# Performance work log

Measured on AMD Instinct MI355X. Metric: run time of the kernel, lower is better.

## Reference

```python
import jax, jax.numpy as jnp
import numpy as np

EPS = 1e-7


def setup_inputs() -> dict:
    key = jax.random.key(0)
    k1, k2, k3, k4 = jax.random.split(key, 4)
    N, M = 8192, 8192
    inputs = jax.random.normal(k1, (N, 2), dtype=jnp.float32)
    outputs = jax.random.normal(k2, (N,), dtype=jnp.float32)
    x = jax.random.normal(k3, (M, 2), dtype=jnp.float32)
    # positive per-query bandwidths in [0.5, 1.5)
    bandwidth = 0.5 + jax.random.uniform(k4, (M,), dtype=jnp.float32)
    return {"x": x, "inputs": inputs, "outputs": outputs, "bandwidth": bandwidth}


def reference(x, inputs, outputs, bandwidth):
    # Squared pairwise distances (cdist followed by .pow(2) in the original):
    # d2[n, m] = ||inputs[n] - x[m]||^2, computed via the expansion to avoid
    # materializing an (N, M, 2) intermediate.
    a2 = jnp.sum(inputs * inputs, axis=1)  # (N,)
    b2 = jnp.sum(x * x, axis=1)            # (M,)
    d2 = a2[:, None] + b2[None, :] - 2.0 * (inputs @ x.T)  # (N, M)
    d2 = jnp.maximum(d2, 0.0)

    bw = bandwidth[None, :]  # (1, M), per-query bandwidth
    weights = jnp.exp(-d2 / (2.0 * bw * bw))  # (N, M)
    # Normalization over dim 0 (over the N reference points)
    weights = weights / (jnp.sum(weights, axis=0, keepdims=True) + EPS)
    # weights.T @ outputs -> (M,), Nadaraya-Watson weighted sum
    weighted = weights.T @ outputs  # (M,)
    return weighted
```

## Files before the change

kernel.cpp:

```cpp
#include <hip/hip_runtime.h>

#define EPS 1e-7f
#define LOG2E 1.44269504088896340736f

constexpr int BLOCK = 1024;
constexpr int JR    = 4;
constexpr int JJ    = 8;
constexpr int JB    = JJ * JR;
constexpr int SS    = BLOCK / JJ;
constexpr int CHUNK = 1024;
constexpr int PTS   = CHUNK / SS;

__global__ __launch_bounds__(BLOCK, 4) void nw_block(
    const float2* __restrict__ x,
    const float2* __restrict__ inputs,
    const float*  __restrict__ outputs,
    const float*  __restrict__ bw,
    float*        __restrict__ out,
    int N, int M)
{
    __shared__ float4 pts[SS][PTS + 1];
    __shared__ float2 red[SS][JB];

    const int tid = threadIdx.x;
    const int jj  = tid & (JJ - 1);
    const int ss  = tid >> 3;

    float c0[JR], c1[JR], c2[JR], c3[JR];
    #pragma unroll
    for (int r = 0; r < JR; ++r) {
        const int j = blockIdx.x * JB + jj + r * JJ;
        if (j < M) {
            float2 xj = x[j];
            float  b  = bw[j];
            float  k  = -LOG2E / (2.0f * b * b);
            c0[r] = k;
            c1[r] = -2.0f * k * xj.x;
            c2[r] = -2.0f * k * xj.y;
            c3[r] = k * fmaf(xj.x, xj.x, xj.y * xj.y);
        } else {
            c0[r] = c1[r] = c2[r] = c3[r] = 0.f;
        }
    }

    float num[JR], den[JR];
    #pragma unroll
    for (int r = 0; r < JR; ++r) { num[r] = 0.f; den[r] = 0.f; }

    float2 pr = make_float2(0.f, 0.f);
    float  po = 0.f;
    if (tid < min(CHUNK, N)) { pr = inputs[tid]; po = outputs[tid]; }

    for (int base = 0; base < N; base += CHUNK) {
        const int cnt = min(CHUNK, N - base);
        if (tid < cnt) {
            pts[tid >> 3][tid & (PTS - 1)] =
                make_float4(pr.x, pr.y, fmaf(pr.x, pr.x, pr.y * pr.y), po);
        } else {
            pts[tid >> 3][tid & (PTS - 1)] =
                make_float4(0.f, 0.f, 3.0e38f, 0.f);
        }
        __syncthreads();

        const int nb = base + CHUNK;
        if (nb < N) {
            const int ncnt = min(CHUNK, N - nb);
            if (tid < ncnt) { pr = inputs[nb + tid]; po = outputs[nb + tid]; }
        }

        const float4* my = pts[ss];
        #pragma unroll
        for (int l = 0; l < PTS; ++l) {
            float4 p = my[l];
            #pragma unroll
            for (int r = 0; r < JR; ++r) {
                float t = fmaf(c0[r], p.z, fmaf(c1[r], p.x, fmaf(c2[r], p.y, c3[r])));
                float w = __builtin_amdgcn_exp2f(t);
                num[r] = fmaf(w, p.w, num[r]);
                den[r] += w;
            }
        }
        __syncthreads();
    }

    #pragma unroll
    for (int r = 0; r < JR; ++r)
        red[ss][jj + r * JJ] = make_float2(num[r], den[r]);
    __syncthreads();
    if (tid < JB) {
        float n = 0.f, d = 0.f;
        for (int s = 0; s < SS; ++s) {
            n += red[s][tid].x;
            d += red[s][tid].y;
        }
        const int jo = blockIdx.x * JB + tid;
        if (jo < M) out[jo] = n / (d + EPS);
    }
}

extern "C" void kernel_launch(void* const* d_in, const int* in_sizes, int n_in,
                              void* d_out, int out_size, void* d_ws, size_t ws_size,
                              hipStream_t stream) {
    const float2* x       = (const float2*)d_in[0];
    const float2* inputs  = (const float2*)d_in[1];
    const float*  outputs = (const float*) d_in[2];
    const float*  bwv     = (const float*) d_in[3];
    const int N = in_sizes[2];
    const int M = in_sizes[3];
    float*        out     = (float*)d_out;

    dim3 grid((M + JB - 1) / JB);
    nw_block<<<grid, BLOCK, 0, stream>>>(x, inputs, outputs, bwv, out, N, M);
}
```

Measured before the change: 75.71 us.

## Use packed f32x2 math with SoA shared layout and smaller blocks

Splits the shared-memory point tile into separate x, y, squared-norm and output arrays so each thread reads pairs of points. The FMA chain and the accumulators then run on 2-wide float vectors, which lets the compiler emit packed FP32 instructions (v_pk_fma_f32). Global loads are widened to float4/float2, each covering two points. The block shrinks to 512 threads with 2 queries per thread, doubling the grid and adding parallelism, but exp2 stays scalar, so transcendental throughput may still cap the gain.

```diff
diff --git a/kernel.cpp b/kernel.cpp
--- a/kernel.cpp
+++ b/kernel.cpp
@@ -3,13 +3,16 @@
 #define EPS 1e-7f
 #define LOG2E 1.44269504088896340736f
 
-constexpr int BLOCK = 1024;
-constexpr int JR    = 4;
+typedef float f32x2 __attribute__((ext_vector_type(2)));
+
+constexpr int BLOCK = 512;
 constexpr int JJ    = 8;
+constexpr int JR    = 2;
 constexpr int JB    = JJ * JR;
 constexpr int SS    = BLOCK / JJ;
 constexpr int CHUNK = 1024;
 constexpr int PTS   = CHUNK / SS;
+constexpr int ROW   = PTS + 2;
 
 __global__ __launch_bounds__(BLOCK, 4) void nw_block(
     const float2* __restrict__ x,
@@ -19,65 +22,87 @@
     float*        __restrict__ out,
     int N, int M)
 {
-    __shared__ float4 pts[SS][PTS + 1];
+    __shared__ __align__(16) float sX[SS][ROW];
+    __shared__ __align__(16) float sY[SS][ROW];
+    __shared__ __align__(16) float sS[SS][ROW];
+    __shared__ __align__(16) float sO[SS][ROW];
     __shared__ float2 red[SS][JB];
 
     const int tid = threadIdx.x;
     const int jj  = tid & (JJ - 1);
     const int ss  = tid >> 3;
 
-    float c0[JR], c1[JR], c2[JR], c3[JR];
+    f32x2 c0p[JR], c1p[JR], c2p[JR], c3p[JR];
     #pragma unroll
     for (int r = 0; r < JR; ++r) {
         const int j = blockIdx.x * JB + jj + r * JJ;
+        float k = 0.f, v1 = 0.f, v2 = 0.f, v3 = 0.f;
         if (j < M) {
             float2 xj = x[j];
             float  b  = bw[j];
-            float  k  = -LOG2E / (2.0f * b * b);
-            c0[r] = k;
-            c1[r] = -2.0f * k * xj.x;
-            c2[r] = -2.0f * k * xj.y;
-            c3[r] = k * fmaf(xj.x, xj.x, xj.y * xj.y);
-        } else {
-            c0[r] = c1[r] = c2[r] = c3[r] = 0.f;
+            k  = -LOG2E / (2.0f * b * b);
+            v1 = -2.0f * k * xj.x;
+            v2 = -2.0f * k * xj.y;
+            v3 = k * fmaf(xj.x, xj.x, xj.y * xj.y);
         }
+        c0p[r] = {k, k}; c1p[r] = {v1, v1}; c2p[r] = {v2, v2}; c3p[r] = {v3, v3};
     }
 
-    float num[JR], den[JR];
+    f32x2 nump[JR], denp[JR];
     #pragma unroll
-    for (int r = 0; r < JR; ++r) { num[r] = 0.f; den[r] = 0.f; }
+    for (int r = 0; r < JR; ++r) { nump[r] = {0.f, 0.f}; denp[r] = {0.f, 0.f}; }
 
-    float2 pr = make_float2(0.f, 0.f);
-    float  po = 0.f;
-    if (tid < min(CHUNK, N)) { pr = inputs[tid]; po = outputs[tid]; }
+    const float4* in4  = (const float4*)inputs;
+    const float2* out2 = (const float2*)outputs;
+    float4 pin  = make_float4(0.f, 0.f, 0.f, 0.f);
+    float2 pout = make_float2(0.f, 0.f);
+    if (2 * tid + 1 < N) { pin = in4[tid]; pout = out2[tid]; }
 
     for (int base = 0; base < N; base += CHUNK) {
         const int cnt = min(CHUNK, N - base);
-        if (tid < cnt) {
-            pts[tid >> 3][tid & (PTS - 1)] =
-                make_float4(pr.x, pr.y, fmaf(pr.x, pr.x, pr.y * pr.y), po);
-        } else {
-            pts[tid >> 3][tid & (PTS - 1)] =
-                make_float4(0.f, 0.f, 3.0e38f, 0.f);
+        {
+            const int  r0 = tid >> 3;
+            const int  s0 = (2 * tid) & (PTS - 1);
+            const bool v0 = (2 * tid) < cnt;
+            const bool v1 = (2 * tid + 1) < cnt;
+            f32x2 xp = {v0 ? pin.x : 0.f, v1 ? pin.z : 0.f};
+            f32x2 yp = {v0 ? pin.y : 0.f, v1 ? pin.w : 0.f};
+            f32x2 sp = {v0 ? fmaf(pin.x, pin.x, pin.y * pin.y) : 3.0e38f,
+                        v1 ? fmaf(pin.z, pin.z, pin.w * pin.w) : 3.0e38f};
+            f32x2 op = {v0 ? pout.x : 0.f, v1 ? pout.y : 0.f};
+            *(f32x2*)&sX[r0][s0] = xp;
+            *(f32x2*)&sY[r0][s0] = yp;
+            *(f32x2*)&sS[r0][s0] = sp;
+            *(f32x2*)&sO[r0][s0] = op;
         }
         __syncthreads();
 
         const int nb = base + CHUNK;
         if (nb < N) {
-            const int ncnt = min(CHUNK, N - nb);
-            if (tid < ncnt) { pr = inputs[nb + tid]; po = outputs[nb + tid]; }
+            const int i0 = (nb >> 1) + tid;
+            if (2 * i0 + 1 < N) { pin = in4[i0]; pout = out2[i0]; }
         }
 
-        const float4* my = pts[ss];
+        const float* mx = sX[ss];
+        const float* my = sY[ss];
+        const float* ms = sS[ss];
+        const float* mo = sO[ss];
         #pragma unroll
-        for (int l = 0; l < PTS; ++l) {
-            float4 p = my[l];
+        for (int m = 0; m < PTS / 2; ++m) {
+            f32x2 xp = *(const f32x2*)&mx[2 * m];
+            f32x2 yp = *(const f32x2*)&my[2 * m];
+            f32x2 sp = *(const f32x2*)&ms[2 * m];
+            f32x2 op = *(const f32x2*)&mo[2 * m];
             #pragma unroll
             for (int r = 0; r < JR; ++r) {
-                float t = fmaf(c0[r], p.z, fmaf(c1[r], p.x, fmaf(c2[r], p.y, c3[r])));
-                float w = __builtin_amdgcn_exp2f(t);
-                num[r] = fmaf(w, p.w, num[r]);
-                den[r] += w;
+                f32x2 t = __builtin_elementwise_fma(c2p[r], yp, c3p[r]);
+                t = __builtin_elementwise_fma(c1p[r], xp, t);
+                t = __builtin_elementwise_fma(c0p[r], sp, t);
+                f32x2 w;
+                w.x = __builtin_amdgcn_exp2f(t.x);
+                w.y = __builtin_amdgcn_exp2f(t.y);
+                nump[r] = __builtin_elementwise_fma(w, op, nump[r]);
+                denp[r] += w;
             }
         }
         __syncthreads();
@@ -85,7 +110,8 @@
 
     #pragma unroll
     for (int r = 0; r < JR; ++r)
-        red[ss][jj + r * JJ] = make_float2(num[r], den[r]);
+        red[ss][jj + r * JJ] = make_float2(nump[r].x + nump[r].y,
+                                           denp[r].x + denp[r].y);
     __syncthreads();
     if (tid < JB) {
         float n = 0.f, d = 0.f;
```

New measurement: 74.12 us. -2.1%, faster.

## Stream reference points via registers with packed FMA and wave-shuffle reduction

Applied to the files above, without the earlier changes.

Replaces the LDS-staged reference-point tiling with a scheme where each thread loads its own reference points straight from global memory into registers. The FMA and accumulate math now uses two-wide float vectors, which can map to packed FP32 instructions. Each block handles 8 queries with 512 threads and reduces partial sums using wave shuffles plus a small LDS step. This removes the LDS traffic and the per-chunk barriers, at the cost of reloading each query's constants and reading more global memory per block, since there are more blocks.

```diff
diff --git a/kernel.cpp b/kernel.cpp
--- a/kernel.cpp
+++ b/kernel.cpp
@@ -3,13 +3,13 @@
 #define EPS 1e-7f
 #define LOG2E 1.44269504088896340736f
 
-constexpr int BLOCK = 1024;
-constexpr int JR    = 4;
-constexpr int JJ    = 8;
-constexpr int JB    = JJ * JR;
-constexpr int SS    = BLOCK / JJ;
-constexpr int CHUNK = 1024;
-constexpr int PTS   = CHUNK / SS;
+typedef float f32x2 __attribute__((ext_vector_type(2)));
+
+constexpr int BLOCK = 512;
+constexpr int PR    = 8;
+constexpr int SEG   = BLOCK * PR * 2;
+constexpr int JT    = 8;
+constexpr int WAVES = BLOCK / 64;
 
 __global__ __launch_bounds__(BLOCK, 4) void nw_block(
     const float2* __restrict__ x,
@@ -19,82 +19,83 @@
     float*        __restrict__ out,
     int N, int M)
 {
-    __shared__ float4 pts[SS][PTS + 1];
-    __shared__ float2 red[SS][JB];
+    __shared__ float2 red[WAVES][JT];
 
-    const int tid = threadIdx.x;
-    const int jj  = tid & (JJ - 1);
-    const int ss  = tid >> 3;
+    const int tid  = threadIdx.x;
+    const int wid  = tid >> 6;
+    const int lane = tid & 63;
+    const int j0   = blockIdx.x * JT;
 
-    float c0[JR], c1[JR], c2[JR], c3[JR];
+    f32x2 nacc[JT], dacc[JT];
     #pragma unroll
-    for (int r = 0; r < JR; ++r) {
-        const int j = blockIdx.x * JB + jj + r * JJ;
-        if (j < M) {
-            float2 xj = x[j];
-            float  b  = bw[j];
-            float  k  = -LOG2E / (2.0f * b * b);
-            c0[r] = k;
-            c1[r] = -2.0f * k * xj.x;
-            c2[r] = -2.0f * k * xj.y;
-            c3[r] = k * fmaf(xj.x, xj.x, xj.y * xj.y);
-        } else {
-            c0[r] = c1[r] = c2[r] = c3[r] = 0.f;
+    for (int jl = 0; jl < JT; ++jl) { nacc[jl] = {0.f, 0.f}; dacc[jl] = {0.f, 0.f}; }
+
+    for (int s0 = 0; s0 < N; s0 += SEG) {
+        f32x2 X2[PR], Y2[PR], S2[PR], O2[PR];
+        #pragma unroll
+        for (int p = 0; p < PR; ++p) {
+            const int ia = s0 + p * BLOCK + tid;
+            const int ib = s0 + (p + PR) * BLOCK + tid;
+            float2 pa = make_float2(0.f, 0.f), pb = make_float2(0.f, 0.f);
+            float  oa = 0.f, ob = 0.f, sa = 3.0e38f, sb = 3.0e38f;
+            if (ia < N) { pa = inputs[ia]; oa = outputs[ia]; sa = fmaf(pa.x, pa.x, pa.y * pa.y); }
+            if (ib < N) { pb = inputs[ib]; ob = outputs[ib]; sb = fmaf(pb.x, pb.x, pb.y * pb.y); }
+            X2[p] = {pa.x, pb.x};
+            Y2[p] = {pa.y, pb.y};
+            S2[p] = {sa,   sb  };
+            O2[p] = {oa,   ob  };
+        }
+
+        #pragma unroll
+        for (int jl = 0; jl < JT; ++jl) {
+            const int j = j0 + jl;
+            float k = 0.f, v1 = 0.f, v2 = 0.f, v3 = 0.f;
+            if (j < M) {
+                float2 xj = x[j];
+                float  b  = bw[j];
+                k  = -LOG2E / (2.0f * b * b);
+                v1 = -2.0f * k * xj.x;
+                v2 = -2.0f * k * xj.y;
+                v3 = k * fmaf(xj.x, xj.x, xj.y * xj.y);
+            }
+            const f32x2 C0 = {k, k}, C1 = {v1, v1}, C2 = {v2, v2}, C3 = {v3, v3};
+            f32x2 n = nacc[jl], d = dacc[jl];
+            #pragma unroll
+            for (int p = 0; p < PR; ++p) {
+                f32x2 t = __builtin_elementwise_fma(C2, Y2[p], C3);
+                t = __builtin_elementwise_fma(C1, X2[p], t);
+                t = __builtin_elementwise_fma(C0, S2[p], t);
+                f32x2 w;
+                w.x = __builtin_amdgcn_exp2f(t.x);
+                w.y = __builtin_amdgcn_exp2f(t.y);
+                n = __builtin_elementwise_fma(w, O2[p], n);
+                d += w;
+            }
+            nacc[jl] = n; dacc[jl] = d;
         }
     }
 
-    float num[JR], den[JR];
     #pragma unroll
-    for (int r = 0; r < JR; ++r) { num[r] = 0.f; den[r] = 0.f; }
-
-    float2 pr = make_float2(0.f, 0.f);
-    float  po = 0.f;
-    if (tid < min(CHUNK, N)) { pr = inputs[tid]; po = outputs[tid]; }
-
-    for (int base = 0; base < N; base += CHUNK) {
-        const int cnt = min(CHUNK, N - base);
-        if (tid < cnt) {
-            pts[tid >> 3][tid & (PTS - 1)] =
-                make_float4(pr.x, pr.y, fmaf(pr.x, pr.x, pr.y * pr.y), po);
-        } else {
-            pts[tid >> 3][tid & (PTS - 1)] =
-                make_float4(0.f, 0.f, 3.0e38f, 0.f);
+    for (int jl = 0; jl < JT; ++jl) {
+        float n = nacc[jl].x + nacc[jl].y;
+        float d = dacc[jl].x + dacc[jl].y;
+        #pragma unroll
+        for (int off = 32; off; off >>= 1) {
+            n += __shfl_xor(n, off);
+            d += __shfl_xor(d, off);
         }
-        __syncthreads();
-
-        const int nb = base + CHUNK;
-        if (nb < N) {
-            const int ncnt = min(CHUNK, N - nb);
-            if (tid < ncnt) { pr = inputs[nb + tid]; po = outputs[nb + tid]; }
+        if (lane == 0) red[wid][jl] = make_float2(n, d);
+    }
+    __syncthreads();
+    if (tid < JT) {
+        float n = 0.f, d = 0.f;
+        #pragma unroll
+        for (int w = 0; w < WAVES; ++w) {
+            n += red[w][tid].x;
+            d += red[w][tid].y;
         }
-
-        const float4* my = pts[ss];
-        #pragma unroll
-        for (int l = 0; l < PTS; ++l) {
-            float4 p = my[l];
-            #pragma unroll
-            for (int r = 0; r < JR; ++r) {
-                float t = fmaf(c0[r], p.z, fmaf(c1[r], p.x, fmaf(c2[r], p.y, c3[r])));
-                float w = __builtin_amdgcn_exp2f(t);
-                num[r] = fmaf(w, p.w, num[r]);
-                den[r] += w;
-            }
-        }
-        __syncthreads();
-    }
-
-    #pragma unroll
-    for (int r = 0; r < JR; ++r)
-        red[ss][jj + r * JJ] = make_float2(num[r], den[r]);
-    __syncthreads();
-    if (tid < JB) {
-        float n = 0.f, d = 0.f;
-        for (int s = 0; s < SS; ++s) {
-            n += red[s][tid].x;
-            d += red[s][tid].y;
-        }
-        const int jo = blockIdx.x * JB + tid;
-        if (jo < M) out[jo] = n / (d + EPS);
+        const int j = j0 + tid;
+        if (j < M) out[j] = n / (d + EPS);
     }
 }
 
@@ -109,6 +110,6 @@
     const int M = in_sizes[3];
     float*        out     = (float*)d_out;
 
-    dim3 grid((M + JB - 1) / JB);
+    dim3 grid((M + JT - 1) / JT);
     nw_block<<<grid, BLOCK, 0, stream>>>(x, inputs, outputs, bwv, out, N, M);
 }
```

Measured after the change: 101.6 us. 34.2% more time.

## Split reference points across blocks with atomic reduction and last-block finalize

Applied to the files above, without the earlier changes.

Each block now handles 256 queries (one per thread) and a 1/32 slice of the reference points. Points are read straight from global memory, with no LDS staging. Partial numerators and denominators are combined with global atomics, and the last block to finish each query group writes the normalized result. This is meant to give more, smaller blocks for better occupancy and to remove the LDS reduction. In exchange it adds a memset, atomics, and per-thread global loads of points, which are broadcast across the wavefront. It also drops the register reuse of each point across several queries.

```diff
diff --git a/kernel.cpp b/kernel.cpp
--- a/kernel.cpp
+++ b/kernel.cpp
@@ -3,13 +3,9 @@
 #define EPS 1e-7f
 #define LOG2E 1.44269504088896340736f
 
-constexpr int BLOCK = 1024;
-constexpr int JR    = 4;
-constexpr int JJ    = 8;
-constexpr int JB    = JJ * JR;
-constexpr int SS    = BLOCK / JJ;
-constexpr int CHUNK = 1024;
-constexpr int PTS   = CHUNK / SS;
+constexpr int BLOCK = 256;
+constexpr int JG_SZ = 256;
+constexpr int NS    = 32;
 
 __global__ __launch_bounds__(BLOCK, 4) void nw_block(
     const float2* __restrict__ x,
@@ -17,84 +13,65 @@
     const float*  __restrict__ outputs,
     const float*  __restrict__ bw,
     float*        __restrict__ out,
-    int N, int M)
+    float*        __restrict__ wsn,
+    float*        __restrict__ wsd,
+    int*          __restrict__ cnt,
+    int N, int M, int JG, int PPS)
 {
-    __shared__ float4 pts[SS][PTS + 1];
-    __shared__ float2 red[SS][JB];
+    __shared__ int lastFlag;
 
     const int tid = threadIdx.x;
-    const int jj  = tid & (JJ - 1);
-    const int ss  = tid >> 3;
+    const int g   = blockIdx.x % JG;
+    const int s   = blockIdx.x / JG;
+    const int j   = g * JG_SZ + tid;
 
-    float c0[JR], c1[JR], c2[JR], c3[JR];
-    #pragma unroll
-    for (int r = 0; r < JR; ++r) {
-        const int j = blockIdx.x * JB + jj + r * JJ;
-        if (j < M) {
-            float2 xj = x[j];
-            float  b  = bw[j];
-            float  k  = -LOG2E / (2.0f * b * b);
-            c0[r] = k;
-            c1[r] = -2.0f * k * xj.x;
-            c2[r] = -2.0f * k * xj.y;
-            c3[r] = k * fmaf(xj.x, xj.x, xj.y * xj.y);
-        } else {
-            c0[r] = c1[r] = c2[r] = c3[r] = 0.f;
-        }
+    float c0 = 0.f, c1 = 0.f, c2 = 0.f, c3 = 0.f;
+    if (j < M) {
+        float2 xj = x[j];
+        float  b  = bw[j];
+        float  k  = -LOG2E / (2.0f * b * b);
+        c0 = k;
+        c1 = -2.0f * k * xj.x;
+        c2 = -2.0f * k * xj.y;
+        c3 = k * fmaf(xj.x, xj.x, xj.y * xj.y);
     }
 
-    float num[JR], den[JR];
-    #pragma unroll
-    for (int r = 0; r < JR; ++r) { num[r] = 0.f; den[r] = 0.f; }
+    const int p0 = s * PPS;
+    const int p1 = min(p0 + PPS, N);
 
-    float2 pr = make_float2(0.f, 0.f);
-    float  po = 0.f;
-    if (tid < min(CHUNK, N)) { pr = inputs[tid]; po = outputs[tid]; }
-
-    for (int base = 0; base < N; base += CHUNK) {
-        const int cnt = min(CHUNK, N - base);
-        if (tid < cnt) {
-            pts[tid >> 3][tid & (PTS - 1)] =
-                make_float4(pr.x, pr.y, fmaf(pr.x, pr.x, pr.y * pr.y), po);
-        } else {
-            pts[tid >> 3][tid & (PTS - 1)] =
-                make_float4(0.f, 0.f, 3.0e38f, 0.f);
-        }
-        __syncthreads();
-
-        const int nb = base + CHUNK;
-        if (nb < N) {
-            const int ncnt = min(CHUNK, N - nb);
-            if (tid < ncnt) { pr = inputs[nb + tid]; po = outputs[nb + tid]; }
-        }
-
-        const float4* my = pts[ss];
-        #pragma unroll
-        for (int l = 0; l < PTS; ++l) {
-            float4 p = my[l];
-            #pragma unroll
-            for (int r = 0; r < JR; ++r) {
-                float t = fmaf(c0[r], p.z, fmaf(c1[r], p.x, fmaf(c2[r], p.y, c3[r])));
-                float w = __builtin_amdgcn_exp2f(t);
-                num[r] = fmaf(w, p.w, num[r]);
-                den[r] += w;
-            }
-        }
-        __syncthreads();
+    float num = 0.f, den = 0.f;
+    #pragma unroll 8
+    for (int p = p0; p < p1; ++p) {
+        const float2 pt = inputs[p];
+        const float  o  = outputs[p];
+        const float A = fmaf(c0, pt.x, c1);
+        const float B = fmaf(c0, pt.y, c2);
+        const float t = fmaf(A, pt.x, fmaf(B, pt.y, c3));
+        const float w = __builtin_amdgcn_exp2f(t);
+        num = fmaf(w, o, num);
+        den += w;
     }
 
-    #pragma unroll
-    for (int r = 0; r < JR; ++r)
-        red[ss][jj + r * JJ] = make_float2(num[r], den[r]);
+    if (j < M) {
+        atomicAdd(&wsn[j], num);
+        atomicAdd(&wsd[j], den);
+    }
+    __threadfence();
     __syncthreads();
-    if (tid < JB) {
-        float n = 0.f, d = 0.f;
-        for (int s = 0; s < SS; ++s) {
-            n += red[s][tid].x;
-            d += red[s][tid].y;
-        }
-        const int jo = blockIdx.x * JB + tid;
-        if (jo < M) out[jo] = n / (d + EPS);
+
+    if (tid == 0) {
+        const int old = __hip_atomic_fetch_add(cnt + g, 1, __ATOMIC_ACQ_REL,
+                                               __HIP_MEMORY_SCOPE_AGENT);
+        lastFlag = (old == NS - 1);
+    }
+    __syncthreads();
+
+    if (lastFlag && j < M) {
+        const float n = __hip_atomic_load(&wsn[j], __ATOMIC_RELAXED,
+                                          __HIP_MEMORY_SCOPE_AGENT);
+        const float d = __hip_atomic_load(&wsd[j], __ATOMIC_RELAXED,
+                                          __HIP_MEMORY_SCOPE_AGENT);
+        out[j] = n / (d + EPS);
     }
 }
 
@@ -109,6 +86,17 @@
     const int M = in_sizes[3];
     float*        out     = (float*)d_out;
 
-    dim3 grid((M + JB - 1) / JB);
-    nw_block<<<grid, BLOCK, 0, stream>>>(x, inputs, outputs, bwv, out, N, M);
+    const int JG  = (M + JG_SZ - 1) / JG_SZ;
+    const int PPS = (N + NS - 1) / NS;
+
+    float* wsn = (float*)d_ws;
+    float* wsd = wsn + M;
+    int*   cnt = (int*)(wsd + M);
+
+    hipMemsetAsync(d_ws, 0, (size_t)(2 * M) * sizeof(float) + (size_t)JG * sizeof(int),
+                   stream);
+
+    dim3 grid(JG * NS);
+    nw_block<<<grid, BLOCK, 0, stream>>>(x, inputs, outputs, bwv, out,
+                                         wsn, wsd, cnt, N, M, JG, PPS);
 }
```

Measured after the change: 147.4 us. 1.95x slower.
